# Kernel tuning notes

Hardware: AMD Instinct MI355X
Metric: run time of the kernel (lower is better)

The kernel has to match this reference:

```python
import jax, jax.numpy as jnp
import numpy as np

B, N, E, F, U = 256, 240, 4338, 28, 100
NEG_SLOPE = 0.2  # PyG GATConv default negative_slope


def setup_inputs() -> dict:
    key = jax.random.key(0)
    ks = jax.random.split(key, 13)
    s = 0.05  # xavier-ish scale
    return {
        "inputs": jax.random.normal(ks[0], (B, N * F), jnp.float32),
        "state": jax.random.normal(ks[1], (B, N * U), jnp.float32),
        "edge_src": jax.random.randint(ks[2], (E,), 0, N, jnp.int32),
        "edge_dst": jax.random.randint(ks[3], (E,), 0, N, jnp.int32),
        # GATConv(U+F -> U): linear weight, attention vectors, output bias
        "Wg": jax.random.normal(ks[4], (U, U + F), jnp.float32) * s,
        "att_src": jax.random.normal(ks[5], (U,), jnp.float32) * s,
        "att_dst": jax.random.normal(ks[6], (U,), jnp.float32) * s,
        "gat_bias": jnp.zeros((U,), jnp.float32),
        # bias_1 added in _gc3 (self.biases[(100,)])
        "bias1": jnp.zeros((U,), jnp.float32),
        # GRU1: GRULinear(100, 200); GRU2: GRULinear(100, 100)
        "W_ru": jax.random.normal(ks[7], (U + F, 2 * U), jnp.float32) * s,
        "b_ru": jnp.zeros((2 * U,), jnp.float32),
        "W_c": jax.random.normal(ks[8], (U + F, U), jnp.float32) * s,
        "b_c": jnp.zeros((U,), jnp.float32),
    }


def _gat_gru(inputs, state, src, dst, Wg, att_src, att_dst, gat_bias, bias1,
             W_ru, b_ru, W_c, b_c):
    xi = inputs.reshape(B, N, F)
    xs = state.reshape(B, N, U)
    # _gc3: concat [state, inputs] -> GATConv per sample (vectorized here)
    x = jnp.concatenate([xs, xi], axis=2)                 # [B, N, U+F]
    h = jnp.einsum("bnf,cf->bnc", x, Wg)                  # [B, N, U]
    a_src = h @ att_src                                    # [B, N]
    a_dst = h @ att_dst                                    # [B, N]
    e = jax.nn.leaky_relu(a_src[:, src] + a_dst[:, dst], NEG_SLOPE)  # [B, E+N]
    eT = e.T                                               # [E+N, B]
    emax = jax.ops.segment_max(eT, dst, num_segments=N)    # [N, B]
    ex = jnp.exp(eT - emax[dst])
    denom = jax.ops.segment_sum(ex, dst, num_segments=N)   # [N, B]
    alpha = ex / denom[dst]                                # [E+N, B]
    msgs = h[:, src].transpose(1, 0, 2) * alpha[:, :, None]  # [E+N, B, U]
    agg = jax.ops.segment_sum(msgs, dst, num_segments=N)   # [N, B, U]
    gstate = agg.transpose(1, 0, 2) + gat_bias + bias1     # [B, N, U]
    st = gstate.reshape(B, N * U)
    # GRU gates (GRULinear concatenates [inputs, hidden] on feature dim)
    cat1 = jnp.concatenate([xi, gstate], axis=2).reshape(-1, U + F)
    ru = jax.nn.sigmoid((cat1 @ W_ru + b_ru).reshape(B, N, 2 * U))
    r = ru[..., :U].reshape(B, N * U)
    u = ru[..., U:].reshape(B, N * U)
    cat2 = jnp.concatenate([xi, (r * st).reshape(B, N, U)], axis=2).reshape(-1, U + F)
    c = jnp.tanh(cat2 @ W_c + b_c).reshape(B, N * U)
    return u * st + (1.0 - u) * c


def reference(inputs, state, edge_src, edge_dst, Wg, att_src, att_dst,
              gat_bias, bias1, W_ru, b_ru, W_c, b_c):
    # PyG GATConv default add_self_loops=True
    loops = jnp.arange(N, dtype=edge_src.dtype)
    src = jnp.concatenate([edge_src, loops])
    dst = jnp.concatenate([edge_dst, loops])
    return _gat_gru(inputs, state, src, dst, Wg, att_src, att_dst, gat_bias,
                    bias1, W_ru, b_ru, W_c, b_c)
```

## Files before the change

kernel.cpp:

```cpp
#include <hip/hip_runtime.h>

#define Bb 256
#define Nn 240
#define Ee 4338
#define Ff 28
#define Uu 100
#define Kk 128
#define Mrows (Bb * Nn)
#define ET (Ee + Nn)
#define AS 136

typedef __attribute__((ext_vector_type(8))) short bf16x8;
typedef __attribute__((ext_vector_type(4))) float f32x4;
typedef unsigned short u16;

__device__ __forceinline__ float bf2f(u16 u) {
  union { unsigned int i; float f; } v; v.i = ((unsigned int)u) << 16; return v.f;
}
__device__ __forceinline__ u16 f2bf(float f) {
  union { float ff; unsigned int i; } v; v.ff = f;
  unsigned int x = v.i;
  return (u16)((x + 0x7fffu + ((x >> 16) & 1u)) >> 16);
}
__device__ __forceinline__ void split4(const float4 v, ushort4& h, ushort4& l) {
  u16 h0 = f2bf(v.x), h1 = f2bf(v.y), h2 = f2bf(v.z), h3 = f2bf(v.w);
  h.x = h0; h.y = h1; h.z = h2; h.w = h3;
  l.x = f2bf(v.x - bf2f(h0)); l.y = f2bf(v.y - bf2f(h1));
  l.z = f2bf(v.z - bf2f(h2)); l.w = f2bf(v.w - bf2f(h3));
}

__global__ __launch_bounds__(256) void k_prep(
    const float* __restrict__ Wg, const float* __restrict__ Wru, const float* __restrict__ Wc,
    u16* __restrict__ wgh, u16* __restrict__ wgl,
    u16* __restrict__ wruh, u16* __restrict__ wrul,
    u16* __restrict__ wch, u16* __restrict__ wcl) {
  int gt = blockIdx.x * 256 + threadIdx.x, GS = gridDim.x * 256;
  for (int i = gt; i < 128 * Kk; i += GS) {
    int c = i >> 7, k = i & 127;
    float v = (c < Uu) ? Wg[c * Kk + k] : 0.f;
    u16 h = f2bf(v); wgh[i] = h; wgl[i] = f2bf(v - bf2f(h));
  }
  for (int i = gt; i < 256 * Kk; i += GS) {
    int n = i >> 7, kp = i & 127;
    int k = (kp < Uu) ? (kp + Ff) : (kp - Uu);
    float v = (n < 2 * Uu) ? Wru[k * (2 * Uu) + n] : 0.f;
    u16 h = f2bf(v); wruh[i] = h; wrul[i] = f2bf(v - bf2f(h));
  }
  for (int i = gt; i < 128 * Kk; i += GS) {
    int n = i >> 7, kp = i & 127;
    int k = (kp < Uu) ? (kp + Ff) : (kp - Uu);
    float v = (n < Uu) ? Wc[k * Uu + n] : 0.f;
    u16 h = f2bf(v); wch[i] = h; wcl[i] = f2bf(v - bf2f(h));
  }
}

__global__ __launch_bounds__(256) void k_csr(
    const int* __restrict__ esrc, const int* __restrict__ edst,
    int* __restrict__ coff, int* __restrict__ cslot) {
  __shared__ int cnt[256];
  __shared__ int scan[256];
  __shared__ int cur[Nn];
  int tid = threadIdx.x;
  cnt[tid] = 0;
  __syncthreads();
  for (int e = tid; e < Ee; e += 256) atomicAdd(&cnt[edst[e]], 1);
  __syncthreads();
  int x = (tid < Nn) ? (cnt[tid] + 1) : 0;
  int incl = x;
  scan[tid] = incl;
  __syncthreads();
#pragma unroll
  for (int d = 1; d < 256; d <<= 1) {
    int t = (tid >= d) ? scan[tid - d] : 0;
    __syncthreads();
    incl += t;
    scan[tid] = incl;
    __syncthreads();
  }
  int excl = incl - x;
  if (tid < Nn) { coff[tid] = excl; cur[tid] = excl; }
  if (tid == 0) coff[Nn] = scan[Nn - 1];
  __syncthreads();
  for (int e = tid; e < Ee; e += 256) {
    int d = edst[e];
    cslot[atomicAdd(&cur[d], 1)] = esrc[e];
  }
  for (int n = tid; n < Nn; n += 256) cslot[atomicAdd(&cur[n], 1)] = n;
}

__global__ __launch_bounds__(1024, 1) void k_fused(
    const float* __restrict__ stt, const float* __restrict__ inp,
    const u16* __restrict__ wgh, const u16* __restrict__ wgl,
    const float* __restrict__ att_s, const float* __restrict__ att_d,
    const int* __restrict__ coff, const int* __restrict__ cslot,
    const float* __restrict__ gbias, const float* __restrict__ b1,
    const u16* __restrict__ wruh, const u16* __restrict__ wrul,
    const float* __restrict__ bru,
    const u16* __restrict__ wch, const u16* __restrict__ wcl,
    const float* __restrict__ bc,
    float* __restrict__ out) {
  __shared__ float hbuf[Nn * Uu];
  __shared__ u16 ahL[32 * AS];
  __shared__ u16 alL[32 * AS];
  __shared__ float gch[32 * Uu];
  __shared__ u16 ugQ[32 * Uu];
  __shared__ float asrcL[Nn];
  __shared__ float adstL[Nn];
  __shared__ int coffL[Nn + 1];
  __shared__ int cslotL[ET];

  int tid = threadIdx.x;
  int b = blockIdx.x;
  const size_t sbase = (size_t)b * Nn * Uu;
  const size_t ibase = (size_t)b * Nn * Ff;

  for (int i = tid; i < Nn + 1; i += 1024) coffL[i] = coff[i];
  for (int i = tid; i < ET; i += 1024) cslotL[i] = cslot[i];
  for (int i = tid; i < Nn; i += 1024) { asrcL[i] = 0.f; adstL[i] = 0.f; }

  int w = tid >> 6, l = tid & 63, l15 = l & 15, q = l >> 4;
  int tile = w & 7, rt0 = w >> 3;
  int cw = tile * 16 + l15;
  int llb = l & 31, half = l >> 5;

  float4 gbv = {0.f, 0.f, 0.f, 0.f};
  if (l < 25) {
    int u0 = l * 4;
    gbv.x = gbias[u0 + 0] + b1[u0 + 0];
    gbv.y = gbias[u0 + 1] + b1[u0 + 1];
    gbv.z = gbias[u0 + 2] + b1[u0 + 2];
    gbv.w = gbias[u0 + 3] + b1[u0 + 3];
  }

  f32x4 zero = {0.f, 0.f, 0.f, 0.f};

  {
    bf16x8 wh[4], wl[4];
#pragma unroll
    for (int s = 0; s < 4; ++s) {
      const int o = cw * Kk + s * 32 + q * 8;
      wh[s] = *(const bf16x8*)(wgh + o);
      wl[s] = *(const bf16x8*)(wgl + o);
    }
    float av = (cw < Uu) ? att_s[cw] : 0.f;
    float dv = (cw < Uu) ? att_d[cw] : 0.f;

    for (int ch0 = 0; ch0 < Nn; ch0 += 32) {
      int rows = Nn - ch0; if (rows > 32) rows = 32;
      bool actrt = (rt0 * 16 < rows);
      for (int j = tid; j < rows * 32; j += 1024) {
        int r = j >> 5, g = j & 31;
        float4 v = (g < 25)
            ? *(const float4*)(stt + sbase + (size_t)(ch0 + r) * Uu + g * 4)
            : *(const float4*)(inp + ibase + (size_t)(ch0 + r) * Ff + (g - 25) * 4);
        ushort4 hh, lo;
        split4(v, hh, lo);
        *(ushort4*)(ahL + r * AS + g * 4) = hh;
        *(ushort4*)(alL + r * AS + g * 4) = lo;
      }
      __syncthreads();
      f32x4 acc = zero;
      if (actrt) {
#pragma unroll
        for (int s = 0; s < 4; ++s) {
          bf16x8 a = *(const bf16x8*)(ahL + (rt0 * 16 + l15) * AS + s * 32 + q * 8);
          bf16x8 bb = *(const bf16x8*)(alL + (rt0 * 16 + l15) * AS + s * 32 + q * 8);
          acc = __builtin_amdgcn_mfma_f32_16x16x32_bf16(a, wh[s], acc, 0, 0, 0);
          acc = __builtin_amdgcn_mfma_f32_16x16x32_bf16(bb, wh[s], acc, 0, 0, 0);
          acc = __builtin_amdgcn_mfma_f32_16x16x32_bf16(a, wl[s], acc, 0, 0, 0);
        }
#pragma unroll
        for (int i = 0; i < 4; ++i) {
          float v = acc[i];
          int row = rt0 * 16 + q * 4 + i;
          if (cw < Uu) hbuf[(ch0 + row) * Uu + cw] = v;
          float va = v * av, vd = v * dv;
#pragma unroll
          for (int msk = 1; msk < 16; msk <<= 1) {
            va += __shfl_xor(va, msk, 64);
            vd += __shfl_xor(vd, msk, 64);
          }
          if (l15 == 0) {
            atomicAdd(&asrcL[ch0 + row], va);
            atomicAdd(&adstL[ch0 + row], vd);
          }
        }
      }
      __syncthreads();
    }
  }

  bf16x8 r0h[4], r0l[4], r1h[4], r1l[4], cch[4], ccl[4];
  int cw1 = 128 + cw;
#pragma unroll
  for (int s = 0; s < 4; ++s) {
    const int o0 = cw * Kk + s * 32 + q * 8;
    const int o1 = cw1 * Kk + s * 32 + q * 8;
    r0h[s] = *(const bf16x8*)(wruh + o0);
    r0l[s] = *(const bf16x8*)(wrul + o0);
    r1h[s] = *(const bf16x8*)(wruh + o1);
    r1l[s] = *(const bf16x8*)(wrul + o1);
    cch[s] = *(const bf16x8*)(wch + o0);
    ccl[s] = *(const bf16x8*)(wcl + o0);
  }
  float bru0 = bru[cw];
  float bru1 = (cw1 < 2 * Uu) ? bru[cw1] : 0.f;
  float bcv = (cw < Uu) ? bc[cw] : 0.f;

  for (int ch0 = 0; ch0 < Nn; ch0 += 32) {
    int rows = Nn - ch0; if (rows > 32) rows = 32;
    bool actrt = (rt0 * 16 < rows);

    for (int n = ch0 + w; n < ch0 + rows; n += 16) {
      int o0 = coffL[n], deg = coffL[n + 1] - o0;
      float ad = adstL[n];
      float ax = 0.f, ay = 0.f, az = 0.f, aw2 = 0.f, den = 0.f;
      for (int c0 = 0; c0 < deg; c0 += 64) {
        int e = c0 + l;
        float we = 0.f; int s = 0;
        if (e < deg) {
          s = cslotL[o0 + e];
          float sc = asrcL[s] + ad;
          sc = (sc > 0.f) ? sc : 0.2f * sc;
          we = __expf(sc);
        }
        float d = we;
#pragma unroll
        for (int msk = 1; msk < 64; msk <<= 1) d += __shfl_xor(d, msk, 64);
        den += d;
        int cn = deg - c0; if (cn > 64) cn = 64;
        for (int e2 = 0; e2 < cn; e2 += 2) {
          int eh = e2 + half;
          float w2 = __shfl(we, eh, 64);
          int s2 = __shfl(s, eh, 64);
          if ((llb < 25) && eh < cn) {
            const float4 hv = *(const float4*)(hbuf + s2 * Uu + llb * 4);
            ax += w2 * hv.x; ay += w2 * hv.y; az += w2 * hv.z; aw2 += w2 * hv.w;
          }
        }
      }
      ax += __shfl_xor(ax, 32, 64);
      ay += __shfl_xor(ay, 32, 64);
      az += __shfl_xor(az, 32, 64);
      aw2 += __shfl_xor(aw2, 32, 64);
      if (l < 25) {
        float inv = 1.f / den;
        float4 o;
        o.x = ax * inv + gbv.x;
        o.y = ay * inv + gbv.y;
        o.z = az * inv + gbv.z;
        o.w = aw2 * inv + gbv.w;
        *(float4*)(gch + (n - ch0) * Uu + l * 4) = o;
      }
    }
    __syncthreads();

    for (int j = tid; j < rows * 32; j += 1024) {
      int r = j >> 5, g = j & 31;
      float4 v = (g < 25)
          ? *(const float4*)(gch + r * Uu + g * 4)
          : *(const float4*)(inp + ibase + (size_t)(ch0 + r) * Ff + (g - 25) * 4);
      ushort4 hh, lo;
      split4(v, hh, lo);
      *(ushort4*)(ahL + r * AS + g * 4) = hh;
      *(ushort4*)(alL + r * AS + g * 4) = lo;
    }
    float sv[4];
    if (actrt) {
#pragma unroll
      for (int i = 0; i < 4; ++i) {
        int row = rt0 * 16 + q * 4 + i;
        sv[i] = (cw < Uu) ? gch[row * Uu + cw] : 0.f;
      }
    }
    __syncthreads();

    float pr[4];
    if (actrt) {
      f32x4 acc = zero;
#pragma unroll
      for (int s = 0; s < 4; ++s) {
        bf16x8 a = *(const bf16x8*)(ahL + (rt0 * 16 + l15) * AS + s * 32 + q * 8);
        bf16x8 bb = *(const bf16x8*)(alL + (rt0 * 16 + l15) * AS + s * 32 + q * 8);
        acc = __builtin_amdgcn_mfma_f32_16x16x32_bf16(a, r0h[s], acc, 0, 0, 0);
        acc = __builtin_amdgcn_mfma_f32_16x16x32_bf16(bb, r0h[s], acc, 0, 0, 0);
        acc = __builtin_amdgcn_mfma_f32_16x16x32_bf16(a, r0l[s], acc, 0, 0, 0);
      }
#pragma unroll
      for (int i = 0; i < 4; ++i) {
        int row = rt0 * 16 + q * 4 + i;
        float y = acc[i] + bru0;
        float g = 1.f / (1.f + __expf(-y));
        if (cw < Uu) pr[i] = g * sv[i];
        else ugQ[row * Uu + (cw - Uu)] = (u16)(g * 65535.f + 0.5f);
      }
      f32x4 acc1 = zero;
#pragma unroll
      for (int s = 0; s < 4; ++s) {
        bf16x8 a = *(const bf16x8*)(ahL + (rt0 * 16 + l15) * AS + s * 32 + q * 8);
        bf16x8 bb = *(const bf16x8*)(alL + (rt0 * 16 + l15) * AS + s * 32 + q * 8);
        acc1 = __builtin_amdgcn_mfma_f32_16x16x32_bf16(a, r1h[s], acc1, 0, 0, 0);
        acc1 = __builtin_amdgcn_mfma_f32_16x16x32_bf16(bb, r1h[s], acc1, 0, 0, 0);
        acc1 = __builtin_amdgcn_mfma_f32_16x16x32_bf16(a, r1l[s], acc1, 0, 0, 0);
      }
#pragma unroll
      for (int i = 0; i < 4; ++i) {
        int row = rt0 * 16 + q * 4 + i;
        float y = acc1[i] + bru1;
        float g = 1.f / (1.f + __expf(-y));
        if (cw1 < 2 * Uu) ugQ[row * Uu + (cw1 - Uu)] = (u16)(g * 65535.f + 0.5f);
      }
    }
    __syncthreads();

    if (actrt) {
#pragma unroll
      for (int i = 0; i < 4; ++i) {
        int row = rt0 * 16 + q * 4 + i;
        if (cw < Uu) {
          float p = pr[i];
          u16 hh = f2bf(p);
          ahL[row * AS + cw] = hh;
          alL[row * AS + cw] = f2bf(p - bf2f(hh));
        }
      }
    }
    __syncthreads();

    if (actrt) {
      f32x4 acc = zero;
#pragma unroll
      for (int s = 0; s < 4; ++s) {
        bf16x8 a = *(const bf16x8*)(ahL + (rt0 * 16 + l15) * AS + s * 32 + q * 8);
        bf16x8 bb = *(const bf16x8*)(alL + (rt0 * 16 + l15) * AS + s * 32 + q * 8);
        acc = __builtin_amdgcn_mfma_f32_16x16x32_bf16(a, cch[s], acc, 0, 0, 0);
        acc = __builtin_amdgcn_mfma_f32_16x16x32_bf16(bb, cch[s], acc, 0, 0, 0);
        acc = __builtin_amdgcn_mfma_f32_16x16x32_bf16(a, ccl[s], acc, 0, 0, 0);
      }
#pragma unroll
      for (int i = 0; i < 4; ++i) {
        int row = rt0 * 16 + q * 4 + i;
        if (cw < Uu) {
          float y = acc[i] + bcv;
          float cv = 1.f - 2.f / (__expf(2.f * y) + 1.f);
          float u = (float)ugQ[row * Uu + cw] * (1.f / 65535.f);
          out[sbase + (size_t)(ch0 + row) * Uu + cw] = u * sv[i] + (1.f - u) * cv;
        }
      }
    }
  }
}

extern "C" void kernel_launch(void* const* d_in, const int* in_sizes, int n_in,
                              void* d_out, int out_size, void* d_ws, size_t ws_size,
                              hipStream_t stream) {
  const float* inp   = (const float*)d_in[0];
  const float* stt   = (const float*)d_in[1];
  const int*   esrc  = (const int*)d_in[2];
  const int*   edst  = (const int*)d_in[3];
  const float* Wg    = (const float*)d_in[4];
  const float* att_s = (const float*)d_in[5];
  const float* att_d = (const float*)d_in[6];
  const float* gbias = (const float*)d_in[7];
  const float* b1    = (const float*)d_in[8];
  const float* Wru   = (const float*)d_in[9];
  const float* bru   = (const float*)d_in[10];
  const float* Wc    = (const float*)d_in[11];
  const float* bc    = (const float*)d_in[12];
  float* out = (float*)d_out;

  char* base = (char*)d_ws;
  size_t o = 0;
  auto alloc = [&](size_t bytes) -> void* {
    void* p = base + o;
    o = (o + bytes + 255) & ~(size_t)255;
    return p;
  };
  u16* wgh  = (u16*)alloc(128 * Kk * sizeof(u16));
  u16* wgl  = (u16*)alloc(128 * Kk * sizeof(u16));
  u16* wruh = (u16*)alloc(256 * Kk * sizeof(u16));
  u16* wrul = (u16*)alloc(256 * Kk * sizeof(u16));
  u16* wch  = (u16*)alloc(128 * Kk * sizeof(u16));
  u16* wcl  = (u16*)alloc(128 * Kk * sizeof(u16));
  int* coff  = (int*)alloc((Nn + 1) * sizeof(int));
  int* cslot = (int*)alloc(ET * sizeof(int));

  k_prep<<<32, 256, 0, stream>>>(Wg, Wru, Wc, wgh, wgl, wruh, wrul, wch, wcl);
  k_csr<<<1, 256, 0, stream>>>(esrc, edst, coff, cslot);
  k_fused<<<Bb, 1024, 0, stream>>>(stt, inp, wgh, wgl, att_s, att_d, coff, cslot,
                                   gbias, b1, wruh, wrul, bru, wch, wcl, bc, out);
}
```

Measured before the change: 253.0 us.

## Merge prep and CSR kernels; reload GRU weights per chunk to cut registers

Merges the weight-split kernel and the CSR-build kernel into a single 33-block launch, removing one kernel launch. In the fused kernel the GRU and candidate weight fragments are no longer held in registers for the whole kernel; they are reloaded from global memory (L2/L1) inside each chunk's MFMA loop, with asm barriers to keep the pointers scalar. The two gate GEMMs are interleaved into one loop that shares the A-operand LDS reads. This cuts register pressure for the 1024-thread block but adds repeated global weight loads on every chunk.

```diff
diff --git a/kernel.cpp b/kernel.cpp
--- a/kernel.cpp
+++ b/kernel.cpp
@@ -29,63 +29,63 @@
   l.z = f2bf(v.z - bf2f(h2)); l.w = f2bf(v.w - bf2f(h3));
 }
 
-__global__ __launch_bounds__(256) void k_prep(
+__global__ __launch_bounds__(256) void k_init(
     const float* __restrict__ Wg, const float* __restrict__ Wru, const float* __restrict__ Wc,
     u16* __restrict__ wgh, u16* __restrict__ wgl,
     u16* __restrict__ wruh, u16* __restrict__ wrul,
-    u16* __restrict__ wch, u16* __restrict__ wcl) {
-  int gt = blockIdx.x * 256 + threadIdx.x, GS = gridDim.x * 256;
-  for (int i = gt; i < 128 * Kk; i += GS) {
-    int c = i >> 7, k = i & 127;
-    float v = (c < Uu) ? Wg[c * Kk + k] : 0.f;
-    u16 h = f2bf(v); wgh[i] = h; wgl[i] = f2bf(v - bf2f(h));
-  }
-  for (int i = gt; i < 256 * Kk; i += GS) {
-    int n = i >> 7, kp = i & 127;
-    int k = (kp < Uu) ? (kp + Ff) : (kp - Uu);
-    float v = (n < 2 * Uu) ? Wru[k * (2 * Uu) + n] : 0.f;
-    u16 h = f2bf(v); wruh[i] = h; wrul[i] = f2bf(v - bf2f(h));
-  }
-  for (int i = gt; i < 128 * Kk; i += GS) {
-    int n = i >> 7, kp = i & 127;
-    int k = (kp < Uu) ? (kp + Ff) : (kp - Uu);
-    float v = (n < Uu) ? Wc[k * Uu + n] : 0.f;
-    u16 h = f2bf(v); wch[i] = h; wcl[i] = f2bf(v - bf2f(h));
-  }
-}
-
-__global__ __launch_bounds__(256) void k_csr(
+    u16* __restrict__ wch, u16* __restrict__ wcl,
     const int* __restrict__ esrc, const int* __restrict__ edst,
     int* __restrict__ coff, int* __restrict__ cslot) {
-  __shared__ int cnt[256];
-  __shared__ int scan[256];
-  __shared__ int cur[Nn];
   int tid = threadIdx.x;
-  cnt[tid] = 0;
-  __syncthreads();
-  for (int e = tid; e < Ee; e += 256) atomicAdd(&cnt[edst[e]], 1);
-  __syncthreads();
-  int x = (tid < Nn) ? (cnt[tid] + 1) : 0;
-  int incl = x;
-  scan[tid] = incl;
-  __syncthreads();
-#pragma unroll
-  for (int d = 1; d < 256; d <<= 1) {
-    int t = (tid >= d) ? scan[tid - d] : 0;
-    __syncthreads();
-    incl += t;
+  if (blockIdx.x < 32) {
+    int gt = blockIdx.x * 256 + tid, GS = 32 * 256;
+    for (int i = gt; i < 128 * Kk; i += GS) {
+      int c = i >> 7, k = i & 127;
+      float v = (c < Uu) ? Wg[c * Kk + k] : 0.f;
+      u16 h = f2bf(v); wgh[i] = h; wgl[i] = f2bf(v - bf2f(h));
+    }
+    for (int i = gt; i < 256 * Kk; i += GS) {
+      int n = i >> 7, kp = i & 127;
+      int k = (kp < Uu) ? (kp + Ff) : (kp - Uu);
+      float v = (n < 2 * Uu) ? Wru[k * (2 * Uu) + n] : 0.f;
+      u16 h = f2bf(v); wruh[i] = h; wrul[i] = f2bf(v - bf2f(h));
+    }
+    for (int i = gt; i < 128 * Kk; i += GS) {
+      int n = i >> 7, kp = i & 127;
+      int k = (kp < Uu) ? (kp + Ff) : (kp - Uu);
+      float v = (n < Uu) ? Wc[k * Uu + n] : 0.f;
+      u16 h = f2bf(v); wch[i] = h; wcl[i] = f2bf(v - bf2f(h));
+    }
+  } else {
+    __shared__ int cnt[256];
+    __shared__ int scan[256];
+    __shared__ int cur[Nn];
+    cnt[tid] = 0;
+    __syncthreads();
+    for (int e = tid; e < Ee; e += 256) atomicAdd(&cnt[edst[e]], 1);
+    __syncthreads();
+    int x = (tid < Nn) ? (cnt[tid] + 1) : 0;
+    int incl = x;
     scan[tid] = incl;
     __syncthreads();
+#pragma unroll
+    for (int d = 1; d < 256; d <<= 1) {
+      int t = (tid >= d) ? scan[tid - d] : 0;
+      __syncthreads();
+      incl += t;
+      scan[tid] = incl;
+      __syncthreads();
+    }
+    int excl = incl - x;
+    if (tid < Nn) { coff[tid] = excl; cur[tid] = excl; }
+    if (tid == 0) coff[Nn] = scan[Nn - 1];
+    __syncthreads();
+    for (int e = tid; e < Ee; e += 256) {
+      int d = edst[e];
+      cslot[atomicAdd(&cur[d], 1)] = esrc[e];
+    }
+    for (int n = tid; n < Nn; n += 256) cslot[atomicAdd(&cur[n], 1)] = n;
   }
-  int excl = incl - x;
-  if (tid < Nn) { coff[tid] = excl; cur[tid] = excl; }
-  if (tid == 0) coff[Nn] = scan[Nn - 1];
-  __syncthreads();
-  for (int e = tid; e < Ee; e += 256) {
-    int d = edst[e];
-    cslot[atomicAdd(&cur[d], 1)] = esrc[e];
-  }
-  for (int n = tid; n < Nn; n += 256) cslot[atomicAdd(&cur[n], 1)] = n;
 }
 
 __global__ __launch_bounds__(1024, 1) void k_fused(
@@ -123,15 +123,6 @@
   int cw = tile * 16 + l15;
   int llb = l & 31, half = l >> 5;
 
-  float4 gbv = {0.f, 0.f, 0.f, 0.f};
-  if (l < 25) {
-    int u0 = l * 4;
-    gbv.x = gbias[u0 + 0] + b1[u0 + 0];
-    gbv.y = gbias[u0 + 1] + b1[u0 + 1];
-    gbv.z = gbias[u0 + 2] + b1[u0 + 2];
-    gbv.w = gbias[u0 + 3] + b1[u0 + 3];
-  }
-
   f32x4 zero = {0.f, 0.f, 0.f, 0.f};
 
   {
@@ -190,22 +181,18 @@
     }
   }
 
-  bf16x8 r0h[4], r0l[4], r1h[4], r1l[4], cch[4], ccl[4];
   int cw1 = 128 + cw;
-#pragma unroll
-  for (int s = 0; s < 4; ++s) {
-    const int o0 = cw * Kk + s * 32 + q * 8;
-    const int o1 = cw1 * Kk + s * 32 + q * 8;
-    r0h[s] = *(const bf16x8*)(wruh + o0);
-    r0l[s] = *(const bf16x8*)(wrul + o0);
-    r1h[s] = *(const bf16x8*)(wruh + o1);
-    r1l[s] = *(const bf16x8*)(wrul + o1);
-    cch[s] = *(const bf16x8*)(wch + o0);
-    ccl[s] = *(const bf16x8*)(wcl + o0);
-  }
   float bru0 = bru[cw];
   float bru1 = (cw1 < 2 * Uu) ? bru[cw1] : 0.f;
   float bcv = (cw < Uu) ? bc[cw] : 0.f;
+  float4 gbv = {0.f, 0.f, 0.f, 0.f};
+  if (l < 25) {
+    int u0 = l * 4;
+    gbv.x = gbias[u0 + 0] + b1[u0 + 0];
+    gbv.y = gbias[u0 + 1] + b1[u0 + 1];
+    gbv.z = gbias[u0 + 2] + b1[u0 + 2];
+    gbv.w = gbias[u0 + 3] + b1[u0 + 3];
+  }
 
   for (int ch0 = 0; ch0 < Nn; ch0 += 32) {
     int rows = Nn - ch0; if (rows > 32) rows = 32;
@@ -275,16 +262,29 @@
     }
     __syncthreads();
 
+    const u16* wruhc = wruh; const u16* wrulc = wrul;
+    asm volatile("" : "+s"(wruhc), "+s"(wrulc));
+
     float pr[4];
     if (actrt) {
-      f32x4 acc = zero;
+      f32x4 acc = zero, acc1 = zero;
 #pragma unroll
       for (int s = 0; s < 4; ++s) {
-        bf16x8 a = *(const bf16x8*)(ahL + (rt0 * 16 + l15) * AS + s * 32 + q * 8);
-        bf16x8 bb = *(const bf16x8*)(alL + (rt0 * 16 + l15) * AS + s * 32 + q * 8);
-        acc = __builtin_amdgcn_mfma_f32_16x16x32_bf16(a, r0h[s], acc, 0, 0, 0);
-        acc = __builtin_amdgcn_mfma_f32_16x16x32_bf16(bb, r0h[s], acc, 0, 0, 0);
-        acc = __builtin_amdgcn_mfma_f32_16x16x32_bf16(a, r0l[s], acc, 0, 0, 0);
+        const int ar = (rt0 * 16 + l15) * AS + s * 32 + q * 8;
+        bf16x8 a = *(const bf16x8*)(ahL + ar);
+        bf16x8 bb = *(const bf16x8*)(alL + ar);
+        const int o0 = cw * Kk + s * 32 + q * 8;
+        const int o1 = cw1 * Kk + s * 32 + q * 8;
+        bf16x8 wh0 = *(const bf16x8*)(wruhc + o0);
+        bf16x8 wl0 = *(const bf16x8*)(wrulc + o0);
+        bf16x8 wh1 = *(const bf16x8*)(wruhc + o1);
+        bf16x8 wl1 = *(const bf16x8*)(wrulc + o1);
+        acc = __builtin_amdgcn_mfma_f32_16x16x32_bf16(a, wh0, acc, 0, 0, 0);
+        acc = __builtin_amdgcn_mfma_f32_16x16x32_bf16(bb, wh0, acc, 0, 0, 0);
+        acc = __builtin_amdgcn_mfma_f32_16x16x32_bf16(a, wl0, acc, 0, 0, 0);
+        acc1 = __builtin_amdgcn_mfma_f32_16x16x32_bf16(a, wh1, acc1, 0, 0, 0);
+        acc1 = __builtin_amdgcn_mfma_f32_16x16x32_bf16(bb, wh1, acc1, 0, 0, 0);
+        acc1 = __builtin_amdgcn_mfma_f32_16x16x32_bf16(a, wl1, acc1, 0, 0, 0);
       }
 #pragma unroll
       for (int i = 0; i < 4; ++i) {
@@ -293,22 +293,9 @@
         float g = 1.f / (1.f + __expf(-y));
         if (cw < Uu) pr[i] = g * sv[i];
         else ugQ[row * Uu + (cw - Uu)] = (u16)(g * 65535.f + 0.5f);
-      }
-      f32x4 acc1 = zero;
-#pragma unroll
-      for (int s = 0; s < 4; ++s) {
-        bf16x8 a = *(const bf16x8*)(ahL + (rt0 * 16 + l15) * AS + s * 32 + q * 8);
-        bf16x8 bb = *(const bf16x8*)(alL + (rt0 * 16 + l15) * AS + s * 32 + q * 8);
-        acc1 = __builtin_amdgcn_mfma_f32_16x16x32_bf16(a, r1h[s], acc1, 0, 0, 0);
-        acc1 = __builtin_amdgcn_mfma_f32_16x16x32_bf16(bb, r1h[s], acc1, 0, 0, 0);
-        acc1 = __builtin_amdgcn_mfma_f32_16x16x32_bf16(a, r1l[s], acc1, 0, 0, 0);
-      }
-#pragma unroll
-      for (int i = 0; i < 4; ++i) {
-        int row = rt0 * 16 + q * 4 + i;
-        float y = acc1[i] + bru1;
-        float g = 1.f / (1.f + __expf(-y));
-        if (cw1 < 2 * Uu) ugQ[row * Uu + (cw1 - Uu)] = (u16)(g * 65535.f + 0.5f);
+        float y1 = acc1[i] + bru1;
+        float g1 = 1.f / (1.f + __expf(-y1));
+        if (cw1 < 2 * Uu) ugQ[row * Uu + (cw1 - Uu)] = (u16)(g1 * 65535.f + 0.5f);
       }
     }
     __syncthreads();
@@ -327,15 +314,21 @@
     }
     __syncthreads();
 
+    const u16* wchc = wch; const u16* wclc = wcl;
+    asm volatile("" : "+s"(wchc), "+s"(wclc));
     if (actrt) {
       f32x4 acc = zero;
 #pragma unroll
       for (int s = 0; s < 4; ++s) {
-        bf16x8 a = *(const bf16x8*)(ahL + (rt0 * 16 + l15) * AS + s * 32 + q * 8);
-        bf16x8 bb = *(const bf16x8*)(alL + (rt0 * 16 + l15) * AS + s * 32 + q * 8);
-        acc = __builtin_amdgcn_mfma_f32_16x16x32_bf16(a, cch[s], acc, 0, 0, 0);
-        acc = __builtin_amdgcn_mfma_f32_16x16x32_bf16(bb, cch[s], acc, 0, 0, 0);
-        acc = __builtin_amdgcn_mfma_f32_16x16x32_bf16(a, ccl[s], acc, 0, 0, 0);
+        const int ar = (rt0 * 16 + l15) * AS + s * 32 + q * 8;
+        bf16x8 a = *(const bf16x8*)(ahL + ar);
+        bf16x8 bb = *(const bf16x8*)(alL + ar);
+        const int o0 = cw * Kk + s * 32 + q * 8;
+        bf16x8 ch_ = *(const bf16x8*)(wchc + o0);
+        bf16x8 cl_ = *(const bf16x8*)(wclc + o0);
+        acc = __builtin_amdgcn_mfma_f32_16x16x32_bf16(a, ch_, acc, 0, 0, 0);
+        acc = __builtin_amdgcn_mfma_f32_16x16x32_bf16(bb, ch_, acc, 0, 0, 0);
+        acc = __builtin_amdgcn_mfma_f32_16x16x32_bf16(a, cl_, acc, 0, 0, 0);
       }
 #pragma unroll
       for (int i = 0; i < 4; ++i) {
@@ -385,8 +378,8 @@
   int* coff  = (int*)alloc((Nn + 1) * sizeof(int));
   int* cslot = (int*)alloc(ET * sizeof(int));
 
-  k_prep<<<32, 256, 0, stream>>>(Wg, Wru, Wc, wgh, wgl, wruh, wrul, wch, wcl);
-  k_csr<<<1, 256, 0, stream>>>(esrc, edst, coff, cslot);
+  k_init<<<33, 256, 0, stream>>>(Wg, Wru, Wc, wgh, wgl, wruh, wrul, wch, wcl,
+                                 esrc, edst, coff, cslot);
   k_fused<<<Bb, 1024, 0, stream>>>(stt, inp, wgh, wgl, att_s, att_d, coff, cslot,
                                    gbias, b1, wruh, wrul, bru, wch, wcl, bc, out);
 }
```

New measurement: 261.1 us. 1.03x slower.
